# Performance work log

Measured on AMD Instinct MI355X. Metric: run time of the kernel, lower is better.

Reference implementation:

```python
import jax, jax.numpy as jnp
import numpy as np

DIM = 256
HEADS = 8
W0, W1 = 8, 8
N = W0 * W1
SCALE = (DIM // HEADS) ** (-0.5)


def _rel_pos_index(w0, w1):
    ch = np.arange(w0)
    cw = np.arange(w1)
    coords = np.stack(np.meshgrid(ch, cw, indexing='ij')).reshape(2, -1)  # (2, N)
    rel = coords[:, :, None] - coords[:, None, :]                          # (2, N, N)
    rel = rel.transpose(1, 2, 0).copy()                                    # (N, N, 2)
    rel[:, :, 0] += w0 - 1
    rel[:, :, 1] += w1 - 1
    rel[:, :, 0] *= 2 * w1 - 1
    return rel.sum(-1)                                                     # (N, N)

REL_IDX = jnp.asarray(_rel_pos_index(W0, W1))


def setup_inputs() -> dict:
    key = jax.random.key(0)
    ks = jax.random.split(key, 9)
    B, C, H, W = 8, DIM, 128, 128
    s = DIM ** -0.5
    return {
        'x': jax.random.normal(ks[0], (B, C, H, W), jnp.float32),
        'embedding': jax.random.normal(ks[1], (1, N, DIM), jnp.float32),
        'rpb_table': jax.random.normal(ks[2], ((2 * W0 - 1) * (2 * W1 - 1), HEADS), jnp.float32),
        'q_w': jax.random.normal(ks[3], (DIM, DIM), jnp.float32) * s,
        'q_b': jnp.zeros((DIM,), jnp.float32),
        'kv_w': jax.random.normal(ks[4], (2 * DIM, DIM), jnp.float32) * s,
        'kv_b': jnp.zeros((2 * DIM,), jnp.float32),
        'proj_w': jax.random.normal(ks[5], (DIM, DIM), jnp.float32) * s,
        'proj_b': jnp.zeros((DIM,), jnp.float32),
    }


def reference(x, embedding, rpb_table, q_w, q_b, kv_w, kv_b, proj_w, proj_b):
    B, C, H, W = x.shape
    # window_partition (faithful to the original, incl. its discarded-permute view):
    # torch views the contiguous (B,C,H,W) buffer as (B, H//w0, w0, W//w1, w1, C)
    win = x.reshape(B, H // W0, W0, W // W1, W1, C)
    win = win.transpose(0, 1, 3, 2, 4, 5).reshape(-1, N, C)  # (Bw, N, C)
    Bw = win.shape[0]
    hd = C // HEADS

    q = jnp.einsum('bnc,dc->bnd', jnp.broadcast_to(embedding, (Bw, N, C)), q_w) + q_b
    q = q.reshape(Bw, N, HEADS, hd).transpose(0, 2, 1, 3)      # (Bw, h, N, hd)
    kv = jnp.einsum('bnc,dc->bnd', win, kv_w) + kv_b           # (Bw, N, 2C)
    kv = kv.reshape(Bw, N, 2, HEADS, hd).transpose(2, 0, 3, 1, 4)
    k, v = kv[0], kv[1]                                         # (Bw, h, N, hd)

    bias = rpb_table[REL_IDX.reshape(-1)].reshape(N, N, HEADS).transpose(2, 0, 1)  # (h, N, N)

    attn = jnp.einsum('bhnd,bhmd->bhnm', q * SCALE, k) + bias[None]
    attn = jax.nn.softmax(attn, axis=-1)
    out = jnp.einsum('bhnm,bhmd->bhnd', attn, v)
    out = out.transpose(0, 2, 1, 3).reshape(Bw, N, C)
    out = jnp.einsum('bnc,dc->bnd', out, proj_w) + proj_b
    return out
```

## Files before the change

### kernel.cpp

```cpp
#include <hip/hip_runtime.h>

typedef short bf16x8 __attribute__((ext_vector_type(8)));
typedef float f32x4 __attribute__((ext_vector_type(4)));
typedef float f32x16 __attribute__((ext_vector_type(16)));
typedef unsigned u32;
typedef unsigned short u16;
typedef unsigned u32x4v __attribute__((ext_vector_type(4)));
typedef unsigned u32x2v __attribute__((ext_vector_type(2)));

union UV { u32x4v u; bf16x8 v; };

__device__ __forceinline__ u16 f2bf(float f){
  u32 u = __float_as_uint(f);
  u += 0x7FFFu + ((u>>16)&1u);
  return (u16)(u>>16);
}
__device__ __forceinline__ u32 pack2(float lo, float hi){
  u32 r;
  asm("v_cvt_pk_bf16_f32 %0, %1, %2" : "=v"(r) : "v"(lo), "v"(hi));
  return r;
}

#define LOG2E 1.4426950408889634f

__global__ void k_qs(const float* __restrict__ emb, const float* __restrict__ q_w,
                     const float* __restrict__ q_b, u16* __restrict__ q_s){
  const int n = blockIdx.x;
  const int d = threadIdx.x;
  const float4* er = (const float4*)(emb + n*256);
  const float4* wr = (const float4*)(q_w + d*256);
  float acc = 0.f;
  for(int c=0;c<64;++c){
    float4 e = er[c], w = wr[c];
    acc += e.x*w.x + e.y*w.y + e.z*w.z + e.w*w.w;
  }
  acc += q_b[d];
  q_s[n*256 + d] = f2bf(acc * (0.17677669529663687f * LOG2E));
}

__global__ void k_bias(const float* __restrict__ rpb, float* __restrict__ bias){
  const int o = blockIdx.x*256 + threadIdx.x;
  const int h = o>>12, n = (o>>6)&63, m = o&63;
  const int idx = ((n>>3)-(m>>3)+7)*15 + ((n&7)-(m&7)+7);
  bias[o] = rpb[idx*8 + h] * LOG2E;
}

__global__ void k_wcvt(const float* __restrict__ kv_w, const float* __restrict__ proj_w,
                       u32* __restrict__ kvb, u32* __restrict__ pjb){
  const int i = blockIdx.x*256 + threadIdx.x;
  if(i < 65536) kvb[i] = pack2(kv_w[2*i], kv_w[2*i+1]);
  else { int j = i - 65536; pjb[j] = pack2(proj_w[2*j], proj_w[2*j+1]); }
}

__global__ __launch_bounds__(512,4) void k_fused(const float* __restrict__ x, const u16* __restrict__ kvw,
                                                 const float* __restrict__ kv_b, const u16* __restrict__ q_s,
                                                 const float* __restrict__ bias, const u16* __restrict__ pjw,
                                                 const float* __restrict__ proj_b, float* __restrict__ out){
  __shared__ char R1[32768];

  const int bw = blockIdx.x;
  const int b = bw>>8, h1 = (bw>>4)&15, w1 = bw&15;
  const int base = b*4194304 + h1*262144 + w1*2048;
  const int tid = threadIdx.x;
  const int w = tid>>6, l = tid&63, g = l>>4, li = l&15;
  const int l31 = l&31, hi = l>>5;

  #pragma unroll
  for(int i=0;i<4;++i){
    int p = i*512 + tid;
    int n = p>>5;
    int c4 = (2*p)&63;
    const float4* gp = (const float4*)(x + base + (n>>3)*32768 + (n&7)*256 + c4*4);
    float4 lo = gp[0], hh = gp[1];
    u32x4v d = { pack2(lo.x,lo.y), pack2(lo.z,lo.w), pack2(hh.x,hh.y), pack2(hh.z,hh.w) };
    *(u32x4v*)(R1 + ((p*16) ^ ((n&7)<<4))) = d;
  }
  __syncthreads();

  f32x4 acc[4][4];
  #pragma unroll
  for(int ct=0;ct<4;++ct){
    float bv = kv_b[w*64 + ct*16 + li];
    #pragma unroll
    for(int rt=0;rt<4;++rt) acc[rt][ct] = (f32x4){bv,bv,bv,bv};
  }
  {
    const u16* wbase = kvw + (w*64 + li)*256 + g*8;
    bf16x8 bcur[4];
    #pragma unroll
    for(int ct=0;ct<4;++ct) bcur[ct] = *(const bf16x8*)(wbase + ct*4096);
    #pragma unroll
    for(int ks=0;ks<8;++ks){
      bf16x8 a[4];
      #pragma unroll
      for(int rt=0;rt<4;++rt){
        int n = rt*16 + li;
        a[rt] = *(const bf16x8*)(R1 + ((n*512 + ks*64 + g*16) ^ ((n&7)<<4)));
      }
      #pragma unroll
      for(int ct=0;ct<4;++ct){
        #pragma unroll
        for(int rt=0;rt<4;++rt)
          acc[rt][ct] = __builtin_amdgcn_mfma_f32_16x16x32_bf16(a[rt], bcur[ct], acc[rt][ct], 0,0,0);
        if(ks<7) bcur[ct] = *(const bf16x8*)(wbase + ct*4096 + (ks+1)*32);
      }
    }
  }
  __syncthreads();

  const int h = w;
  bf16x8 qf[2][2];
  #pragma unroll
  for(int nt=0;nt<2;++nt)
    #pragma unroll
    for(int ks=0;ks<2;++ks)
      qf[nt][ks] = *(const bf16x8*)(q_s + (nt*32 + l31)*256 + h*32 + ks*16 + hi*8);

  const int oddl = li & 1;
  if(w < 4){
    #pragma unroll
    for(int ct=0;ct<4;++ct){
      int colp = w*64 + ct*16 + (li & ~1);
      #pragma unroll
      for(int rt=0;rt<4;++rt){
        float v0=acc[rt][ct][0], v1=acc[rt][ct][1], v2=acc[rt][ct][2], v3=acc[rt][ct][3];
        float o0=__shfl_xor(v0,1), o1=__shfl_xor(v1,1), o2=__shfl_xor(v2,1), o3=__shfl_xor(v3,1);
        u32 d0 = oddl ? pack2(o2,v2) : pack2(v0,o0);
        u32 d1 = oddl ? pack2(o3,v3) : pack2(v1,o1);
        int row0 = rt*16 + 4*g + (oddl ? 2 : 0);
        *(u32*)(R1 + ((row0*512     + colp*2) ^ ((row0&7)<<4)))     = d0;
        *(u32*)(R1 + (((row0+1)*512 + colp*2) ^ (((row0+1)&7)<<4))) = d1;
      }
    }
  }
  __syncthreads();

  bf16x8 kf[2][2];
  #pragma unroll
  for(int mt=0;mt<2;++mt)
    #pragma unroll
    for(int ks=0;ks<2;++ks){
      int row = mt*32 + l31;
      kf[mt][ks] = *(const bf16x8*)(R1 + ((row*512 + (h*32 + ks*16 + hi*8)*2) ^ ((row&7)<<4)));
    }
  __syncthreads();

  if(w >= 4){
    #pragma unroll
    for(int ct=0;ct<4;++ct){
      int c2 = (w-4)*64 + ct*16 + li;
      int hv = c2>>5, e = c2&31;
      #pragma unroll
      for(int rt=0;rt<4;++rt){
        u32x2v d;
        d[0] = pack2(acc[rt][ct][0], acc[rt][ct][1]);
        d[1] = pack2(acc[rt][ct][2], acc[rt][ct][3]);
        int m0 = rt*16 + 4*g;
        *(u32x2v*)(R1 + (((hv*32 + e)*128 + m0*2) ^ ((e&7)<<4))) = d;
      }
    }
  }
  __syncthreads();

  f32x16 S[2][2];
  #pragma unroll
  for(int mt=0;mt<2;++mt)
    #pragma unroll
    for(int nt=0;nt<2;++nt){
      int n = nt*32 + l31;
      const float* bp = bias + h*4096 + n*64 + mt*32 + 4*hi;
      #pragma unroll
      for(int q=0;q<4;++q){
        float4 bv = *(const float4*)(bp + q*8);
        S[mt][nt][4*q+0] = bv.x; S[mt][nt][4*q+1] = bv.y;
        S[mt][nt][4*q+2] = bv.z; S[mt][nt][4*q+3] = bv.w;
      }
    }
  #pragma unroll
  for(int ks=0;ks<2;++ks)
    #pragma unroll
    for(int mt=0;mt<2;++mt)
      #pragma unroll
      for(int nt=0;nt<2;++nt)
        S[mt][nt] = __builtin_amdgcn_mfma_f32_32x32x16_bf16(kf[mt][ks], qf[nt][ks], S[mt][nt], 0,0,0);

  float rs[2];
  u32 cb0[2][8], cb1[2][8];
  #pragma unroll
  for(int nt=0;nt<2;++nt){
    float t[16];
    #pragma unroll
    for(int j=0;j<16;++j) t[j] = fmaxf(S[0][nt][j], S[1][nt][j]);
    #pragma unroll
    for(int s=8;s>0;s>>=1)
      #pragma unroll
      for(int j=0;j<8;++j) if(j<s) t[j] = fmaxf(t[j], t[j+s]);
    float mx = fmaxf(t[0], __shfl_xor(t[0], 32));
    float sm[16];
    #pragma unroll
    for(int j=0;j<16;++j){
      S[0][nt][j] = __builtin_amdgcn_exp2f(S[0][nt][j] - mx);
      S[1][nt][j] = __builtin_amdgcn_exp2f(S[1][nt][j] - mx);
      sm[j] = S[0][nt][j] + S[1][nt][j];
    }
    #pragma unroll
    for(int s=8;s>0;s>>=1)
      #pragma unroll
      for(int j=0;j<8;++j) if(j<s) sm[j] += sm[j+s];
    float total = sm[0] + __shfl_xor(sm[0], 32);
    rs[nt] = 1.0f/total;
    #pragma unroll
    for(int mt=0;mt<2;++mt)
      #pragma unroll
      for(int q=0;q<4;++q){
        cb0[nt][mt*4+q] = pack2(S[mt][nt][4*q+0], S[mt][nt][4*q+1]);
        cb1[nt][mt*4+q] = pack2(S[mt][nt][4*q+2], S[mt][nt][4*q+3]);
      }
  }

  f32x16 O[2];
  O[0] = (f32x16)(0.f); O[1] = (f32x16)(0.f);
  #pragma unroll
  for(int ks2=0;ks2<4;++ks2){
    bf16x8 vf = *(const bf16x8*)(R1 + (((h*32 + l31)*128 + (ks2*16 + hi*8)*2) ^ ((l31&7)<<4)));
    #pragma unroll
    for(int nt=0;nt<2;++nt){
      u32 A0 = cb0[nt][2*ks2], B0 = cb0[nt][2*ks2+1];
      u32 A1 = cb1[nt][2*ks2], B1 = cb1[nt][2*ks2+1];
      u32 r0 = (u32)__shfl_xor((int)(hi ? A0 : B0), 32);
      u32 r1 = (u32)__shfl_xor((int)(hi ? A1 : B1), 32);
      u32 w0 = hi ? r0 : A0;
      u32 w1 = hi ? r1 : A1;
      u32 w2 = hi ? B0 : r0;
      u32 w3 = hi ? B1 : r1;
      UV t; t.u = (u32x4v){w0,w1,w2,w3};
      O[nt] = __builtin_amdgcn_mfma_f32_32x32x16_bf16(vf, t.v, O[nt], 0,0,0);
    }
  }

  #pragma unroll
  for(int nt=0;nt<2;++nt){
    int n = nt*32 + l31;
    #pragma unroll
    for(int q=0;q<4;++q){
      u32x2v d;
      d[0] = pack2(O[nt][4*q+0]*rs[nt], O[nt][4*q+1]*rs[nt]);
      d[1] = pack2(O[nt][4*q+2]*rs[nt], O[nt][4*q+3]*rs[nt]);
      *(u32x2v*)(R1 + h*4096 + ((n*64 + (8*q + 4*hi)*2) ^ ((n&7)<<4))) = d;
    }
  }
  __syncthreads();

  {
    f32x4 pacc[4][2];
    #pragma unroll
    for(int ct=0;ct<2;++ct){
      float bv = proj_b[w*32 + ct*16 + li];
      #pragma unroll
      for(int rt=0;rt<4;++rt) pacc[rt][ct] = (f32x4){bv,bv,bv,bv};
    }
    const u16* pbase = pjw + (w*32 + li)*256 + g*8;
    bf16x8 bc[2];
    #pragma unroll
    for(int ct=0;ct<2;++ct) bc[ct] = *(const bf16x8*)(pbase + ct*4096);
    #pragma unroll
    for(int ks=0;ks<8;++ks){
      bf16x8 a[4];
      #pragma unroll
      for(int rt=0;rt<4;++rt){
        int row = rt*16 + li;
        a[rt] = *(const bf16x8*)(R1 + ks*4096 + ((row*64 + g*16) ^ ((row&7)<<4)));
      }
      #pragma unroll
      for(int ct=0;ct<2;++ct){
        #pragma unroll
        for(int rt=0;rt<4;++rt)
          pacc[rt][ct] = __builtin_amdgcn_mfma_f32_16x16x32_bf16(a[rt], bc[ct], pacc[rt][ct], 0,0,0);
        if(ks<7) bc[ct] = *(const bf16x8*)(pbase + ct*4096 + (ks+1)*32);
      }
    }
    #pragma unroll
    for(int rt=0;rt<4;++rt)
      #pragma unroll
      for(int ct=0;ct<2;++ct)
        #pragma unroll
        for(int r=0;r<4;++r)
          out[(bw*64 + rt*16 + 4*g + r)*256 + w*32 + ct*16 + li] = pacc[rt][ct][r];
  }
}

extern "C" void kernel_launch(void* const* d_in, const int* in_sizes, int n_in,
                              void* d_out, int out_size, void* d_ws, size_t ws_size,
                              hipStream_t stream){
  (void)in_sizes; (void)n_in; (void)out_size;
  const float* x      = (const float*)d_in[0];
  const float* emb    = (const float*)d_in[1];
  const float* rpb    = (const float*)d_in[2];
  const float* q_w    = (const float*)d_in[3];
  const float* q_b    = (const float*)d_in[4];
  const float* kv_w   = (const float*)d_in[5];
  const float* kv_b   = (const float*)d_in[6];
  const float* proj_w = (const float*)d_in[7];
  const float* proj_b = (const float*)d_in[8];
  float* out = (float*)d_out;

  char* ws = (char*)d_ws;
  if(ws_size < (size_t)557056) return;
  u16* q_s   = (u16*)(ws);
  float* bias= (float*)(ws + 32768);
  u32* kvb   = (u32*)(ws + 163840);
  u32* pjb   = (u32*)(ws + 425984);

  k_qs   <<<  64, 256, 0, stream>>>(emb, q_w, q_b, q_s);
  k_bias <<< 128, 256, 0, stream>>>(rpb, bias);
  k_wcvt <<< 384, 256, 0, stream>>>(kv_w, proj_w, kvb, pjb);
  k_fused<<<2048, 512, 0, stream>>>(x, (const u16*)kvb, kv_b, q_s, bias,
                                    (const u16*)pjb, proj_b, out);
}
```

Measured before the change: 360.5 us.

## Process two windows per block with double-buffered LDS and merge prep kernels

The three small prep kernels are merged into one launch to cut launch overhead. The fused kernel now handles two windows per block, using 64KB of shared memory split into an x/K region and a V/output region. It prefetches the next window's x into LDS during the projection GEMM of the current window, and it drops one barrier by placing K and V in separate buffers. The trade-off is double the LDS per block, which lowers occupancy (with 160KB LDS per CU, likely 2 blocks instead of 4), and half as many blocks in the grid.

New measurement: 680.8 us. +88.9%, slower.

```diff
diff --git a/kernel.cpp b/kernel.cpp
--- a/kernel.cpp
+++ b/kernel.cpp
@@ -23,269 +23,282 @@
 
 #define LOG2E 1.4426950408889634f
 
-__global__ void k_qs(const float* __restrict__ emb, const float* __restrict__ q_w,
-                     const float* __restrict__ q_b, u16* __restrict__ q_s){
-  const int n = blockIdx.x;
-  const int d = threadIdx.x;
-  const float4* er = (const float4*)(emb + n*256);
-  const float4* wr = (const float4*)(q_w + d*256);
-  float acc = 0.f;
-  for(int c=0;c<64;++c){
-    float4 e = er[c], w = wr[c];
-    acc += e.x*w.x + e.y*w.y + e.z*w.z + e.w*w.w;
+__global__ void k_prep(const float* __restrict__ emb, const float* __restrict__ q_w,
+                       const float* __restrict__ q_b, u16* __restrict__ q_s,
+                       const float* __restrict__ rpb, float* __restrict__ bias,
+                       const float* __restrict__ kv_w, const float* __restrict__ proj_w,
+                       u32* __restrict__ kvb, u32* __restrict__ pjb){
+  const int blk = blockIdx.x, tid = threadIdx.x;
+  if(blk < 64){
+    const int n = blk, d = tid;
+    const float4* er = (const float4*)(emb + n*256);
+    const float4* wr = (const float4*)(q_w + d*256);
+    float acc = 0.f;
+    for(int c=0;c<64;++c){
+      float4 e = er[c], w = wr[c];
+      acc += e.x*w.x + e.y*w.y + e.z*w.z + e.w*w.w;
+    }
+    acc += q_b[d];
+    q_s[n*256 + d] = f2bf(acc * (0.17677669529663687f * LOG2E));
+  } else if(blk < 192){
+    const int o = (blk-64)*256 + tid;
+    const int h = o>>12, n = (o>>6)&63, m = o&63;
+    const int idx = ((n>>3)-(m>>3)+7)*15 + ((n&7)-(m&7)+7);
+    bias[o] = rpb[idx*8 + h] * LOG2E;
+  } else {
+    const int i = (blk-192)*256 + tid;
+    if(i < 65536) kvb[i] = pack2(kv_w[2*i], kv_w[2*i+1]);
+    else { int j = i - 65536; pjb[j] = pack2(proj_w[2*j], proj_w[2*j+1]); }
   }
-  acc += q_b[d];
-  q_s[n*256 + d] = f2bf(acc * (0.17677669529663687f * LOG2E));
-}
-
-__global__ void k_bias(const float* __restrict__ rpb, float* __restrict__ bias){
-  const int o = blockIdx.x*256 + threadIdx.x;
-  const int h = o>>12, n = (o>>6)&63, m = o&63;
-  const int idx = ((n>>3)-(m>>3)+7)*15 + ((n&7)-(m&7)+7);
-  bias[o] = rpb[idx*8 + h] * LOG2E;
-}
-
-__global__ void k_wcvt(const float* __restrict__ kv_w, const float* __restrict__ proj_w,
-                       u32* __restrict__ kvb, u32* __restrict__ pjb){
-  const int i = blockIdx.x*256 + threadIdx.x;
-  if(i < 65536) kvb[i] = pack2(kv_w[2*i], kv_w[2*i+1]);
-  else { int j = i - 65536; pjb[j] = pack2(proj_w[2*j], proj_w[2*j+1]); }
-}
-
-__global__ __launch_bounds__(512,4) void k_fused(const float* __restrict__ x, const u16* __restrict__ kvw,
-                                                 const float* __restrict__ kv_b, const u16* __restrict__ q_s,
-                                                 const float* __restrict__ bias, const u16* __restrict__ pjw,
-                                                 const float* __restrict__ proj_b, float* __restrict__ out){
-  __shared__ char R1[32768];
-
-  const int bw = blockIdx.x;
-  const int b = bw>>8, h1 = (bw>>4)&15, w1 = bw&15;
-  const int base = b*4194304 + h1*262144 + w1*2048;
-  const int tid = threadIdx.x;
-  const int w = tid>>6, l = tid&63, g = l>>4, li = l&15;
-  const int l31 = l&31, hi = l>>5;
-
+}
+
+__device__ __forceinline__ void stage_x(const float* __restrict__ xb, char* RA, int tid){
   #pragma unroll
   for(int i=0;i<4;++i){
     int p = i*512 + tid;
     int n = p>>5;
     int c4 = (2*p)&63;
-    const float4* gp = (const float4*)(x + base + (n>>3)*32768 + (n&7)*256 + c4*4);
+    const float4* gp = (const float4*)(xb + (n>>3)*32768 + (n&7)*256 + c4*4);
     float4 lo = gp[0], hh = gp[1];
     u32x4v d = { pack2(lo.x,lo.y), pack2(lo.z,lo.w), pack2(hh.x,hh.y), pack2(hh.z,hh.w) };
-    *(u32x4v*)(R1 + ((p*16) ^ ((n&7)<<4))) = d;
+    *(u32x4v*)(RA + ((p*16) ^ ((n&7)<<4))) = d;
+  }
+}
+
+__global__ __launch_bounds__(512,4) void k_fused(const float* __restrict__ x, const u16* __restrict__ kvw,
+                                                 const float* __restrict__ kv_b, const u16* __restrict__ q_s,
+                                                 const float* __restrict__ bias, const u16* __restrict__ pjw,
+                                                 const float* __restrict__ proj_b, float* __restrict__ out){
+  __shared__ char smem[65536];
+  char* RA = smem;
+  char* RB = smem + 32768;
+
+  const int tid = threadIdx.x;
+  const int w = tid>>6, l = tid&63, g = l>>4, li = l&15;
+  const int l31 = l&31, hi = l>>5;
+  const int h = w;
+  const int oddl = li & 1;
+
+  const int vw = blockIdx.x*2;
+  {
+    const int b=vw>>8, h1=(vw>>4)&15, w1=vw&15;
+    stage_x(x + b*4194304 + h1*262144 + w1*2048, RA, tid);
   }
   __syncthreads();
 
-  f32x4 acc[4][4];
-  #pragma unroll
-  for(int ct=0;ct<4;++ct){
-    float bv = kv_b[w*64 + ct*16 + li];
-    #pragma unroll
-    for(int rt=0;rt<4;++rt) acc[rt][ct] = (f32x4){bv,bv,bv,bv};
-  }
-  {
-    const u16* wbase = kvw + (w*64 + li)*256 + g*8;
-    bf16x8 bcur[4];
-    #pragma unroll
-    for(int ct=0;ct<4;++ct) bcur[ct] = *(const bf16x8*)(wbase + ct*4096);
-    #pragma unroll
-    for(int ks=0;ks<8;++ks){
-      bf16x8 a[4];
-      #pragma unroll
-      for(int rt=0;rt<4;++rt){
-        int n = rt*16 + li;
-        a[rt] = *(const bf16x8*)(R1 + ((n*512 + ks*64 + g*16) ^ ((n&7)<<4)));
-      }
+  #pragma unroll 1
+  for(int wi=0; wi<2; ++wi){
+    const int bw = vw + wi;
+
+    f32x4 acc[4][4];
+    #pragma unroll
+    for(int ct=0;ct<4;++ct){
+      float bv = kv_b[w*64 + ct*16 + li];
+      #pragma unroll
+      for(int rt=0;rt<4;++rt) acc[rt][ct] = (f32x4){bv,bv,bv,bv};
+    }
+    {
+      const u16* wbase = kvw + (w*64 + li)*256 + g*8;
+      bf16x8 bcur[4];
+      #pragma unroll
+      for(int ct=0;ct<4;++ct) bcur[ct] = *(const bf16x8*)(wbase + ct*4096);
+      #pragma unroll
+      for(int ks=0;ks<8;++ks){
+        bf16x8 a[4];
+        #pragma unroll
+        for(int rt=0;rt<4;++rt){
+          int n = rt*16 + li;
+          a[rt] = *(const bf16x8*)(RA + ((n*512 + ks*64 + g*16) ^ ((n&7)<<4)));
+        }
+        #pragma unroll
+        for(int ct=0;ct<4;++ct){
+          #pragma unroll
+          for(int rt=0;rt<4;++rt)
+            acc[rt][ct] = __builtin_amdgcn_mfma_f32_16x16x32_bf16(a[rt], bcur[ct], acc[rt][ct], 0,0,0);
+          if(ks<7) bcur[ct] = *(const bf16x8*)(wbase + ct*4096 + (ks+1)*32);
+        }
+      }
+    }
+    __syncthreads();
+
+    if(w < 4){
       #pragma unroll
       for(int ct=0;ct<4;++ct){
-        #pragma unroll
-        for(int rt=0;rt<4;++rt)
-          acc[rt][ct] = __builtin_amdgcn_mfma_f32_16x16x32_bf16(a[rt], bcur[ct], acc[rt][ct], 0,0,0);
-        if(ks<7) bcur[ct] = *(const bf16x8*)(wbase + ct*4096 + (ks+1)*32);
-      }
-    }
-  }
-  __syncthreads();
-
-  const int h = w;
-  bf16x8 qf[2][2];
-  #pragma unroll
-  for(int nt=0;nt<2;++nt)
+        int colp = w*64 + ct*16 + (li & ~1);
+        #pragma unroll
+        for(int rt=0;rt<4;++rt){
+          float v0=acc[rt][ct][0], v1=acc[rt][ct][1], v2=acc[rt][ct][2], v3=acc[rt][ct][3];
+          float o0=__shfl_xor(v0,1), o1=__shfl_xor(v1,1), o2=__shfl_xor(v2,1), o3=__shfl_xor(v3,1);
+          u32 d0 = oddl ? pack2(o2,v2) : pack2(v0,o0);
+          u32 d1 = oddl ? pack2(o3,v3) : pack2(v1,o1);
+          int row0 = rt*16 + 4*g + (oddl ? 2 : 0);
+          *(u32*)(RA + ((row0*512     + colp*2) ^ ((row0&7)<<4)))     = d0;
+          *(u32*)(RA + (((row0+1)*512 + colp*2) ^ (((row0+1)&7)<<4))) = d1;
+        }
+      }
+    } else {
+      #pragma unroll
+      for(int ct=0;ct<4;++ct){
+        int c2 = (w-4)*64 + ct*16 + li;
+        int hv = c2>>5, e = c2&31;
+        #pragma unroll
+        for(int rt=0;rt<4;++rt){
+          u32x2v d;
+          d[0] = pack2(acc[rt][ct][0], acc[rt][ct][1]);
+          d[1] = pack2(acc[rt][ct][2], acc[rt][ct][3]);
+          int m0 = rt*16 + 4*g;
+          *(u32x2v*)(RB + (((hv*32 + e)*128 + m0*2) ^ ((e&7)<<4))) = d;
+        }
+      }
+    }
+    __syncthreads();
+
+    bf16x8 qf[2][2], kf[2][2];
+    #pragma unroll
+    for(int nt=0;nt<2;++nt)
+      #pragma unroll
+      for(int ks=0;ks<2;++ks)
+        qf[nt][ks] = *(const bf16x8*)(q_s + (nt*32 + l31)*256 + h*32 + ks*16 + hi*8);
+    #pragma unroll
+    for(int mt=0;mt<2;++mt)
+      #pragma unroll
+      for(int ks=0;ks<2;++ks){
+        int row = mt*32 + l31;
+        kf[mt][ks] = *(const bf16x8*)(RA + ((row*512 + (h*32 + ks*16 + hi*8)*2) ^ ((row&7)<<4)));
+      }
+
+    f32x16 S[2][2];
+    #pragma unroll
+    for(int mt=0;mt<2;++mt)
+      #pragma unroll
+      for(int nt=0;nt<2;++nt){
+        int n = nt*32 + l31;
+        const float* bp = bias + h*4096 + n*64 + mt*32 + 4*hi;
+        #pragma unroll
+        for(int q=0;q<4;++q){
+          float4 bv = *(const float4*)(bp + q*8);
+          S[mt][nt][4*q+0] = bv.x; S[mt][nt][4*q+1] = bv.y;
+          S[mt][nt][4*q+2] = bv.z; S[mt][nt][4*q+3] = bv.w;
+        }
+      }
     #pragma unroll
     for(int ks=0;ks<2;++ks)
-      qf[nt][ks] = *(const bf16x8*)(q_s + (nt*32 + l31)*256 + h*32 + ks*16 + hi*8);
-
-  const int oddl = li & 1;
-  if(w < 4){
-    #pragma unroll
-    for(int ct=0;ct<4;++ct){
-      int colp = w*64 + ct*16 + (li & ~1);
-      #pragma unroll
-      for(int rt=0;rt<4;++rt){
-        float v0=acc[rt][ct][0], v1=acc[rt][ct][1], v2=acc[rt][ct][2], v3=acc[rt][ct][3];
-        float o0=__shfl_xor(v0,1), o1=__shfl_xor(v1,1), o2=__shfl_xor(v2,1), o3=__shfl_xor(v3,1);
-        u32 d0 = oddl ? pack2(o2,v2) : pack2(v0,o0);
-        u32 d1 = oddl ? pack2(o3,v3) : pack2(v1,o1);
-        int row0 = rt*16 + 4*g + (oddl ? 2 : 0);
-        *(u32*)(R1 + ((row0*512     + colp*2) ^ ((row0&7)<<4)))     = d0;
-        *(u32*)(R1 + (((row0+1)*512 + colp*2) ^ (((row0+1)&7)<<4))) = d1;
-      }
-    }
-  }
-  __syncthreads();
-
-  bf16x8 kf[2][2];
-  #pragma unroll
-  for(int mt=0;mt<2;++mt)
-    #pragma unroll
-    for(int ks=0;ks<2;++ks){
-      int row = mt*32 + l31;
-      kf[mt][ks] = *(const bf16x8*)(R1 + ((row*512 + (h*32 + ks*16 + hi*8)*2) ^ ((row&7)<<4)));
-    }
-  __syncthreads();
-
-  if(w >= 4){
-    #pragma unroll
-    for(int ct=0;ct<4;++ct){
-      int c2 = (w-4)*64 + ct*16 + li;
-      int hv = c2>>5, e = c2&31;
-      #pragma unroll
-      for(int rt=0;rt<4;++rt){
-        u32x2v d;
-        d[0] = pack2(acc[rt][ct][0], acc[rt][ct][1]);
-        d[1] = pack2(acc[rt][ct][2], acc[rt][ct][3]);
-        int m0 = rt*16 + 4*g;
-        *(u32x2v*)(R1 + (((hv*32 + e)*128 + m0*2) ^ ((e&7)<<4))) = d;
-      }
-    }
-  }
-  __syncthreads();
-
-  f32x16 S[2][2];
-  #pragma unroll
-  for(int mt=0;mt<2;++mt)
+      #pragma unroll
+      for(int mt=0;mt<2;++mt)
+        #pragma unroll
+        for(int nt=0;nt<2;++nt)
+          S[mt][nt] = __builtin_amdgcn_mfma_f32_32x32x16_bf16(kf[mt][ks], qf[nt][ks], S[mt][nt], 0,0,0);
+
+    float rs[2];
+    u32 cb0[2][8], cb1[2][8];
+    #pragma unroll
+    for(int nt=0;nt<2;++nt){
+      float t[16];
+      #pragma unroll
+      for(int j=0;j<16;++j) t[j] = fmaxf(S[0][nt][j], S[1][nt][j]);
+      #pragma unroll
+      for(int s=8;s>0;s>>=1)
+        #pragma unroll
+        for(int j=0;j<8;++j) if(j<s) t[j] = fmaxf(t[j], t[j+s]);
+      float mx = fmaxf(t[0], __shfl_xor(t[0], 32));
+      float sm[16];
+      #pragma unroll
+      for(int j=0;j<16;++j){
+        S[0][nt][j] = __builtin_amdgcn_exp2f(S[0][nt][j] - mx);
+        S[1][nt][j] = __builtin_amdgcn_exp2f(S[1][nt][j] - mx);
+        sm[j] = S[0][nt][j] + S[1][nt][j];
+      }
+      #pragma unroll
+      for(int s=8;s>0;s>>=1)
+        #pragma unroll
+        for(int j=0;j<8;++j) if(j<s) sm[j] += sm[j+s];
+      float total = sm[0] + __shfl_xor(sm[0], 32);
+      rs[nt] = 1.0f/total;
+      #pragma unroll
+      for(int mt=0;mt<2;++mt)
+        #pragma unroll
+        for(int q=0;q<4;++q){
+          cb0[nt][mt*4+q] = pack2(S[mt][nt][4*q+0], S[mt][nt][4*q+1]);
+          cb1[nt][mt*4+q] = pack2(S[mt][nt][4*q+2], S[mt][nt][4*q+3]);
+        }
+    }
+
+    f32x16 O[2];
+    O[0] = (f32x16)(0.f); O[1] = (f32x16)(0.f);
+    #pragma unroll
+    for(int ks2=0;ks2<4;++ks2){
+      bf16x8 vf = *(const bf16x8*)(RB + (((h*32 + l31)*128 + (ks2*16 + hi*8)*2) ^ ((l31&7)<<4)));
+      #pragma unroll
+      for(int nt=0;nt<2;++nt){
+        u32 A0 = cb0[nt][2*ks2], B0 = cb0[nt][2*ks2+1];
+        u32 A1 = cb1[nt][2*ks2], B1 = cb1[nt][2*ks2+1];
+        u32 r0 = (u32)__shfl_xor((int)(hi ? A0 : B0), 32);
+        u32 r1 = (u32)__shfl_xor((int)(hi ? A1 : B1), 32);
+        u32 w0 = hi ? r0 : A0;
+        u32 w1 = hi ? r1 : A1;
+        u32 w2 = hi ? B0 : r0;
+        u32 w3 = hi ? B1 : r1;
+        UV t; t.u = (u32x4v){w0,w1,w2,w3};
+        O[nt] = __builtin_amdgcn_mfma_f32_32x32x16_bf16(vf, t.v, O[nt], 0,0,0);
+      }
+    }
+
     #pragma unroll
     for(int nt=0;nt<2;++nt){
       int n = nt*32 + l31;
-      const float* bp = bias + h*4096 + n*64 + mt*32 + 4*hi;
       #pragma unroll
       for(int q=0;q<4;++q){
-        float4 bv = *(const float4*)(bp + q*8);
-        S[mt][nt][4*q+0] = bv.x; S[mt][nt][4*q+1] = bv.y;
-        S[mt][nt][4*q+2] = bv.z; S[mt][nt][4*q+3] = bv.w;
-      }
-    }
-  #pragma unroll
-  for(int ks=0;ks<2;++ks)
-    #pragma unroll
-    for(int mt=0;mt<2;++mt)
-      #pragma unroll
-      for(int nt=0;nt<2;++nt)
-        S[mt][nt] = __builtin_amdgcn_mfma_f32_32x32x16_bf16(kf[mt][ks], qf[nt][ks], S[mt][nt], 0,0,0);
-
-  float rs[2];
-  u32 cb0[2][8], cb1[2][8];
-  #pragma unroll
-  for(int nt=0;nt<2;++nt){
-    float t[16];
-    #pragma unroll
-    for(int j=0;j<16;++j) t[j] = fmaxf(S[0][nt][j], S[1][nt][j]);
-    #pragma unroll
-    for(int s=8;s>0;s>>=1)
-      #pragma unroll
-      for(int j=0;j<8;++j) if(j<s) t[j] = fmaxf(t[j], t[j+s]);
-    float mx = fmaxf(t[0], __shfl_xor(t[0], 32));
-    float sm[16];
-    #pragma unroll
-    for(int j=0;j<16;++j){
-      S[0][nt][j] = __builtin_amdgcn_exp2f(S[0][nt][j] - mx);
-      S[1][nt][j] = __builtin_amdgcn_exp2f(S[1][nt][j] - mx);
-      sm[j] = S[0][nt][j] + S[1][nt][j];
-    }
-    #pragma unroll
-    for(int s=8;s>0;s>>=1)
-      #pragma unroll
-      for(int j=0;j<8;++j) if(j<s) sm[j] += sm[j+s];
-    float total = sm[0] + __shfl_xor(sm[0], 32);
-    rs[nt] = 1.0f/total;
-    #pragma unroll
-    for(int mt=0;mt<2;++mt)
-      #pragma unroll
-      for(int q=0;q<4;++q){
-        cb0[nt][mt*4+q] = pack2(S[mt][nt][4*q+0], S[mt][nt][4*q+1]);
-        cb1[nt][mt*4+q] = pack2(S[mt][nt][4*q+2], S[mt][nt][4*q+3]);
-      }
-  }
-
-  f32x16 O[2];
-  O[0] = (f32x16)(0.f); O[1] = (f32x16)(0.f);
-  #pragma unroll
-  for(int ks2=0;ks2<4;++ks2){
-    bf16x8 vf = *(const bf16x8*)(R1 + (((h*32 + l31)*128 + (ks2*16 + hi*8)*2) ^ ((l31&7)<<4)));
-    #pragma unroll
-    for(int nt=0;nt<2;++nt){
-      u32 A0 = cb0[nt][2*ks2], B0 = cb0[nt][2*ks2+1];
-      u32 A1 = cb1[nt][2*ks2], B1 = cb1[nt][2*ks2+1];
-      u32 r0 = (u32)__shfl_xor((int)(hi ? A0 : B0), 32);
-      u32 r1 = (u32)__shfl_xor((int)(hi ? A1 : B1), 32);
-      u32 w0 = hi ? r0 : A0;
-      u32 w1 = hi ? r1 : A1;
-      u32 w2 = hi ? B0 : r0;
-      u32 w3 = hi ? B1 : r1;
-      UV t; t.u = (u32x4v){w0,w1,w2,w3};
-      O[nt] = __builtin_amdgcn_mfma_f32_32x32x16_bf16(vf, t.v, O[nt], 0,0,0);
-    }
-  }
-
-  #pragma unroll
-  for(int nt=0;nt<2;++nt){
-    int n = nt*32 + l31;
-    #pragma unroll
-    for(int q=0;q<4;++q){
-      u32x2v d;
-      d[0] = pack2(O[nt][4*q+0]*rs[nt], O[nt][4*q+1]*rs[nt]);
-      d[1] = pack2(O[nt][4*q+2]*rs[nt], O[nt][4*q+3]*rs[nt]);
-      *(u32x2v*)(R1 + h*4096 + ((n*64 + (8*q + 4*hi)*2) ^ ((n&7)<<4))) = d;
-    }
-  }
-  __syncthreads();
-
-  {
-    f32x4 pacc[4][2];
-    #pragma unroll
-    for(int ct=0;ct<2;++ct){
-      float bv = proj_b[w*32 + ct*16 + li];
-      #pragma unroll
-      for(int rt=0;rt<4;++rt) pacc[rt][ct] = (f32x4){bv,bv,bv,bv};
-    }
-    const u16* pbase = pjw + (w*32 + li)*256 + g*8;
-    bf16x8 bc[2];
-    #pragma unroll
-    for(int ct=0;ct<2;++ct) bc[ct] = *(const bf16x8*)(pbase + ct*4096);
-    #pragma unroll
-    for(int ks=0;ks<8;++ks){
-      bf16x8 a[4];
-      #pragma unroll
-      for(int rt=0;rt<4;++rt){
-        int row = rt*16 + li;
-        a[rt] = *(const bf16x8*)(R1 + ks*4096 + ((row*64 + g*16) ^ ((row&7)<<4)));
-      }
+        u32x2v d;
+        d[0] = pack2(O[nt][4*q+0]*rs[nt], O[nt][4*q+1]*rs[nt]);
+        d[1] = pack2(O[nt][4*q+2]*rs[nt], O[nt][4*q+3]*rs[nt]);
+        *(u32x2v*)(RB + h*4096 + ((n*64 + (8*q + 4*hi)*2) ^ ((n&7)<<4))) = d;
+      }
+    }
+    __syncthreads();
+
+    if(wi==0){
+      const int vn = vw+1;
+      const int b=vn>>8, h1=(vn>>4)&15, w1=vn&15;
+      stage_x(x + b*4194304 + h1*262144 + w1*2048, RA, tid);
+    }
+
+    {
+      f32x4 pacc[4][2];
       #pragma unroll
       for(int ct=0;ct<2;++ct){
-        #pragma unroll
-        for(int rt=0;rt<4;++rt)
-          pacc[rt][ct] = __builtin_amdgcn_mfma_f32_16x16x32_bf16(a[rt], bc[ct], pacc[rt][ct], 0,0,0);
-        if(ks<7) bc[ct] = *(const bf16x8*)(pbase + ct*4096 + (ks+1)*32);
-      }
-    }
-    #pragma unroll
-    for(int rt=0;rt<4;++rt)
-      #pragma unroll
-      for(int ct=0;ct<2;++ct)
-        #pragma unroll
-        for(int r=0;r<4;++r)
-          out[(bw*64 + rt*16 + 4*g + r)*256 + w*32 + ct*16 + li] = pacc[rt][ct][r];
+        float bv = proj_b[w*32 + ct*16 + li];
+        #pragma unroll
+        for(int rt=0;rt<4;++rt) pacc[rt][ct] = (f32x4){bv,bv,bv,bv};
+      }
+      const u16* pbase = pjw + (w*32 + li)*256 + g*8;
+      bf16x8 bc[2];
+      #pragma unroll
+      for(int ct=0;ct<2;++ct) bc[ct] = *(const bf16x8*)(pbase + ct*4096);
+      #pragma unroll
+      for(int ks=0;ks<8;++ks){
+        bf16x8 a[4];
+        #pragma unroll
+        for(int rt=0;rt<4;++rt){
+          int row = rt*16 + li;
+          a[rt] = *(const bf16x8*)(RB + ks*4096 + ((row*64 + g*16) ^ ((row&7)<<4)));
+        }
+        #pragma unroll
+        for(int ct=0;ct<2;++ct){
+          #pragma unroll
+          for(int rt=0;rt<4;++rt)
+            pacc[rt][ct] = __builtin_amdgcn_mfma_f32_16x16x32_bf16(a[rt], bc[ct], pacc[rt][ct], 0,0,0);
+          if(ks<7) bc[ct] = *(const bf16x8*)(pbase + ct*4096 + (ks+1)*32);
+        }
+      }
+      #pragma unroll
+      for(int rt=0;rt<4;++rt)
+        #pragma unroll
+        for(int ct=0;ct<2;++ct)
+          #pragma unroll
+          for(int r=0;r<4;++r)
+            out[(bw*64 + rt*16 + 4*g + r)*256 + w*32 + ct*16 + li] = pacc[rt][ct][r];
+    }
+    if(wi==0) __syncthreads();
   }
 }
 
@@ -311,9 +324,7 @@
   u32* kvb   = (u32*)(ws + 163840);
   u32* pjb   = (u32*)(ws + 425984);
 
-  k_qs   <<<  64, 256, 0, stream>>>(emb, q_w, q_b, q_s);
-  k_bias <<< 128, 256, 0, stream>>>(rpb, bias);
-  k_wcvt <<< 384, 256, 0, stream>>>(kv_w, proj_w, kvb, pjb);
-  k_fused<<<2048, 512, 0, stream>>>(x, (const u16*)kvb, kv_b, q_s, bias,
+  k_prep <<< 576, 256, 0, stream>>>(emb, q_w, q_b, q_s, rpb, bias, kv_w, proj_w, kvb, pjb);
+  k_fused<<<1024, 512, 0, stream>>>(x, (const u16*)kvb, kv_b, q_s, bias,
                                     (const u16*)pjb, proj_b, out);
 }
```
